# Performance work log

Hardware: AMD Instinct MI355X
Metric: run time of the kernel (lower is better)

The kernel has to match this reference:

```python
import jax, jax.numpy as jnp
import numpy as np

N_NODES = 100000
N_EDGES = 1600000
C = 128          # in_channels
H = 32           # hidden MLP width
D = 1            # Dirichlet concentration dims
T = 3            # Taylor params (estimate_bpr=True)
JITTER = 1e-20


def gcn_conv(x, W, b, edge_index, n_nodes):
    """PyG GCNConv: add self-loops, symmetric normalization, aggregate to target."""
    h = x @ W                                   # [N, C] transform first (smaller than gathering raw x then transforming per-edge)
    src = jnp.concatenate([edge_index[0], jnp.arange(n_nodes)])
    dst = jnp.concatenate([edge_index[1], jnp.arange(n_nodes)])
    deg = jax.ops.segment_sum(jnp.ones_like(dst, dtype=h.dtype), dst, num_segments=n_nodes)
    dinv = jnp.where(deg > 0, jax.lax.rsqrt(deg), 0.0)
    norm = dinv[src] * dinv[dst]                # [E+N]
    msg = h[src] * norm[:, None]                # gather + scale  [E+N, C]
    out = jax.ops.segment_sum(msg, dst, num_segments=n_nodes)  # scatter-add
    return out + b


def setup_inputs() -> dict:
    key = jax.random.key(0)
    ks = jax.random.split(key, 20)
    s = 1.0 / np.sqrt(C)
    sh = 1.0 / np.sqrt(H)
    x = jax.random.normal(ks[0], (N_NODES, C), dtype=jnp.float32)
    edge_index = jax.random.randint(ks[1], (2, N_EDGES), 0, N_NODES)
    p = {
        "x": x, "edge_index": edge_index,
        # actor params
        "a_conv_W": jax.random.uniform(ks[2], (C, C), jnp.float32, -s, s),
        "a_conv_b": jnp.zeros((C,), jnp.float32),
        "a_l1_W": jax.random.uniform(ks[3], (C, H), jnp.float32, -s, s),
        "a_l1_b": jax.random.uniform(ks[4], (H,), jnp.float32, -s, s),
        "a_l2_W": jax.random.uniform(ks[5], (H, H), jnp.float32, -sh, sh),
        "a_l2_b": jax.random.uniform(ks[6], (H,), jnp.float32, -sh, sh),
        "a_l3_W": jax.random.uniform(ks[7], (H, D + T), jnp.float32, -sh, sh),
        "a_l3_b": jax.random.uniform(ks[8], (D + T,), jnp.float32, -sh, sh),
        # critic params
        "c_conv_W": jax.random.uniform(ks[9], (C, C), jnp.float32, -s, s),
        "c_conv_b": jnp.zeros((C,), jnp.float32),
        "c_l1_W": jax.random.uniform(ks[10], (C, H), jnp.float32, -s, s),
        "c_l1_b": jax.random.uniform(ks[11], (H,), jnp.float32, -s, s),
        "c_l2_W": jax.random.uniform(ks[12], (H, H), jnp.float32, -sh, sh),
        "c_l2_b": jax.random.uniform(ks[13], (H,), jnp.float32, -sh, sh),
        "c_l3_W": jax.random.uniform(ks[14], (H, 1), jnp.float32, -sh, sh),
        "c_l3_b": jax.random.uniform(ks[15], (1,), jnp.float32, -sh, sh),
    }
    return p


def reference(x, edge_index,
              a_conv_W, a_conv_b, a_l1_W, a_l1_b, a_l2_W, a_l2_b, a_l3_W, a_l3_b,
              c_conv_W, c_conv_b, c_l1_W, c_l1_b, c_l2_W, c_l2_b, c_l3_W, c_l3_b):
    n = x.shape[0]
    # ---- actor (GNNActor.forward) ----
    a = jax.nn.relu(gcn_conv(x, a_conv_W, a_conv_b, edge_index, n)) + x   # residual
    a = jax.nn.relu(a @ a_l1_W + a_l1_b)
    a = jax.nn.relu(a @ a_l2_W + a_l2_b)
    a_out = a @ a_l3_W + a_l3_b                      # [N, D+T]
    concentration = jax.nn.softplus(a_out[:, :D]).reshape(-1) + JITTER
    taylor_params = jax.nn.softplus(a_out[:, D:]) + JITTER
    # ---- critic (GNNCritic.forward) ----
    c = jax.nn.relu(gcn_conv(x, c_conv_W, c_conv_b, edge_index, n)) + x
    c = jnp.sum(c, axis=0)                           # graph readout [C]
    c = jax.nn.relu(c @ c_l1_W + c_l1_b)
    c = jax.nn.relu(c @ c_l2_W + c_l2_b)
    value = c @ c_l3_W + c_l3_b                      # [1]
    return concentration, taylor_params, value
```

## Files before the change

### kernel.cpp

```cpp
#include <hip/hip_runtime.h>
#include <math.h>

#define CCH 128
#define HID 32
#define SLOTS 64
#define NBINS 391
#define BSHIFT 8
#define BCAP 4608

typedef __attribute__((ext_vector_type(8))) short bf16x8;
typedef __attribute__((ext_vector_type(4))) float f32x4;

__device__ __forceinline__ unsigned bf16pk(float a, float b) {
    unsigned ua = __builtin_bit_cast(unsigned, a);
    unsigned ub = __builtin_bit_cast(unsigned, b);
    ua = (ua + 0x7FFFu + ((ua >> 16) & 1u)) >> 16;
    ub = (ub + 0x7FFFu + ((ub >> 16) & 1u)) >> 16;
    return ua | (ub << 16);
}
__device__ __forceinline__ unsigned short bf16s(float a) {
    unsigned ua = __builtin_bit_cast(unsigned, a);
    ua = (ua + 0x7FFFu + ((ua >> 16) & 1u)) >> 16;
    return (unsigned short)ua;
}
__device__ __forceinline__ float bflo(unsigned v) {
    return __builtin_bit_cast(float, v << 16);
}
__device__ __forceinline__ float bfhi(unsigned v) {
    return __builtin_bit_cast(float, v & 0xFFFF0000u);
}

__global__ void k_zero(float* __restrict__ csum, int* __restrict__ binCnt) {
    int t = threadIdx.x;
    if (t < CCH) csum[t] = 0.f;
    for (int i = t; i < NBINS; i += 256) binCnt[i] = 0;
}

__global__ __launch_bounds__(256, 4)
void k_bin(const int* __restrict__ ei, int E,
           int* __restrict__ binCnt, unsigned* __restrict__ stage) {
    int t = threadIdx.x;
    __shared__ int lcnt[NBINS];
    __shared__ int lofs[NBINS];
    const int nchunk = (E + 2047) / 2048;
    for (int ch = blockIdx.x; ch < nchunk; ch += gridDim.x) {
        int base = ch * 2048;
        for (int i = t; i < NBINS; i += 256) lcnt[i] = 0;
        __syncthreads();
        unsigned pk[8]; int bin[8];
#pragma unroll
        for (int k = 0; k < 8; k++) {
            int e = base + k * 256 + t;
            if (e < E) {
                unsigned src = (unsigned)ei[e];
                unsigned dst = (unsigned)ei[E + e];
                bin[k] = dst >> BSHIFT;
                pk[k] = src | ((dst & 0xFFu) << 17);
                atomicAdd(&lcnt[bin[k]], 1);
            } else bin[k] = -1;
        }
        __syncthreads();
        for (int i = t; i < NBINS; i += 256) {
            int c = lcnt[i];
            lofs[i] = c ? atomicAdd(&binCnt[i], c) : 0;
        }
        __syncthreads();
#pragma unroll
        for (int k = 0; k < 8; k++) {
            if (bin[k] >= 0) {
                int pos = atomicAdd(&lofs[bin[k]], 1);
                if (pos < BCAP)
                    stage[(long)bin[k] * BCAP + pos] = pk[k];
            }
        }
        __syncthreads();
    }
}

__global__ __launch_bounds__(256)
void k_place(const unsigned* __restrict__ stage, const int* __restrict__ binCnt,
             int* __restrict__ cnt, int* __restrict__ csr) {
    __shared__ int lcnt[256];
    __shared__ int lofs[256];
    __shared__ int lcur[256];
    __shared__ int wtot[4];
    __shared__ unsigned ssrc[BCAP];
    __shared__ unsigned short sd8[BCAP];

    int t = threadIdx.x;
    int b = blockIdx.x;
    int count = binCnt[b];
    if (count > BCAP) count = BCAP;
    const unsigned* sp = stage + (long)b * BCAP;
    int dbase = b << BSHIFT;

    lcnt[t] = 0;
    __syncthreads();
    for (int i = t; i < count; i += 256)
        atomicAdd(&lcnt[sp[i] >> 17], 1);
    __syncthreads();

    int craw = lcnt[t];
    int cc = craw > SLOTS ? SLOTS : craw;
    int lane = t & 63, wv = t >> 6;
    int x = cc;
#pragma unroll
    for (int d = 1; d < 64; d <<= 1) {
        int y = __shfl_up(x, d, 64);
        if (lane >= d) x += y;
    }
    if (lane == 63) wtot[wv] = x;
    __syncthreads();
    int pre = 0;
#pragma unroll
    for (int k = 0; k < 4; k++) pre += (k < wv) ? wtot[k] : 0;
    int excl = pre + x - cc;
    lofs[t] = excl;
    lcur[t] = excl;
    int total = wtot[0] + wtot[1] + wtot[2] + wtot[3];
    __syncthreads();

    for (int i = t; i < count; i += 256) {
        unsigned p = sp[i];
        int d8 = (int)(p >> 17);
        int pos = atomicAdd(&lcur[d8], 1);
        if (pos - lofs[d8] < SLOTS) {
            ssrc[pos] = (p & 0x1FFFFu) << 5;
            sd8[pos] = (unsigned short)d8;
        }
    }
    __syncthreads();

    for (int i = t; i < total; i += 256) {
        int d8 = sd8[i];
        csr[(long)(dbase + d8) * SLOTS + (i - lofs[d8])] = (int)ssrc[i];
    }
    cnt[dbase + t] = craw;
}

__global__ __launch_bounds__(256, 4)
void k_prep(const float* __restrict__ aW, const float* __restrict__ cW,
            const float* __restrict__ x, const int* __restrict__ cnt,
            unsigned short* __restrict__ Wt, unsigned short* __restrict__ xsb,
            float* __restrict__ csum, int N) {
    __shared__ float scs[CCH];
    int t = threadIdx.x;
    int id = blockIdx.x * 256 + t;
    if (id < 32768) {
        int conv = id >> 14;
        int rem = id & 16383;
        int n = rem >> 7;
        int k = rem & 127;
        const float* W = conv ? cW : aW;
        Wt[id] = bf16s(W[k * CCH + n]);
    }
    if (blockIdx.x == 0 && t < 64) ((unsigned*)xsb)[(long)N * 64 + t] = 0u;

    const int n4 = N * 32;
    float c0 = 0.f, c1 = 0.f, c2 = 0.f, c3 = 0.f;
    const float4* x4 = (const float4*)x;
    uint2* xo = (uint2*)xsb;
    int stride = gridDim.x * 256;
    for (int i = id; i < n4; i += stride) {
        int node = i >> 5;
        float dv = rsqrtf((float)cnt[node] + 1.0f);
        float4 v = x4[i];
        c0 += v.x; c1 += v.y; c2 += v.z; c3 += v.w;
        uint2 p;
        p.x = bf16pk(dv * v.x, dv * v.y);
        p.y = bf16pk(dv * v.z, dv * v.w);
        xo[i] = p;
    }
    if (t < CCH) scs[t] = 0.f;
    __syncthreads();
    int c4 = (t & 31) * 4;
    atomicAdd(&scs[c4 + 0], c0);
    atomicAdd(&scs[c4 + 1], c1);
    atomicAdd(&scs[c4 + 2], c2);
    atomicAdd(&scs[c4 + 3], c3);
    __syncthreads();
    if (t < CCH) atomicAdd(&csum[t], scs[t]);
}

__global__ __launch_bounds__(256, 4)
void k_gather_y(const unsigned short* __restrict__ xs,
                const int* __restrict__ cnt,
                const int* __restrict__ csr,
                unsigned short* __restrict__ yb, int N) {
    int t = threadIdx.x;
    int lane = t & 63;
    int wid = t >> 6;
    int half = lane >> 5;
    int hl = lane & 31;
    int wg = blockIdx.x * 4 + wid;
    int stride = gridDim.x * 4;
    const uint2* xu = (const uint2*)xs;
    uint2* yu = (uint2*)yb;
    int npairs = N >> 1;
    int zoff = N << 5;

    for (int p = wg; p < npairs; p += stride) {
        int nA = p * 2;
        int degr = cnt[nA + half];
        float dvd = rsqrtf((float)degr + 1.0f);
        int deg = degr > SLOTS ? SLOTS : degr;
        int degA = __builtin_amdgcn_readlane(deg, 0);
        int degB = __builtin_amdgcn_readlane(deg, 32);
        int dmax = degA > degB ? degA : degB;
        dmax = __builtin_amdgcn_readfirstlane(dmax);

        int idxl = csr[(long)nA * SLOTS + lane + (lane & 32)];
        if (hl >= deg) idxl = zoff;

        uint2 vs = xu[(long)nA * 32 + lane];

        uint2 v[32];
#pragma unroll
        for (int e = 0; e < 32; e++) {
            int iA = __builtin_amdgcn_readlane(idxl, e);
            int iB = __builtin_amdgcn_readlane(idxl, 32 + e);
            int boff = half ? iB : iA;
            v[e] = xu[boff + hl];
        }

        float a0 = bflo(vs.x), a1 = bfhi(vs.x);
        float a2 = bflo(vs.y), a3 = bfhi(vs.y);
#pragma unroll
        for (int e = 0; e < 32; e++) {
            a0 += bflo(v[e].x);
            a1 += __builtin_bit_cast(float, v[e].x);
            a2 += bflo(v[e].y);
            a3 += __builtin_bit_cast(float, v[e].y);
        }

        if (dmax > 32) {
            int idxh = csr[(long)nA * SLOTS + lane + (lane & 32) + 32];
            if (hl + 32 >= deg) idxh = zoff;
            int dx8 = (dmax + 7) & ~7;
            for (int e = 32; e < dx8; e += 8) {
                uint2 w[8];
#pragma unroll
                for (int k = 0; k < 8; k++) {
                    int iA = __builtin_amdgcn_readlane(idxh, e - 32 + k);
                    int iB = __builtin_amdgcn_readlane(idxh, e + k);
                    int boff = half ? iB : iA;
                    w[k] = xu[boff + hl];
                }
#pragma unroll
                for (int k = 0; k < 8; k++) {
                    a0 += bflo(w[k].x);
                    a1 += __builtin_bit_cast(float, w[k].x);
                    a2 += bflo(w[k].y);
                    a3 += __builtin_bit_cast(float, w[k].y);
                }
            }
        }
        uint2 o;
        o.x = bf16pk(dvd * a0, dvd * a1);
        o.y = bf16pk(dvd * a2, dvd * a3);
        yu[(long)nA * 32 + lane] = o;
    }
}

__global__ __launch_bounds__(256, 4)
void k_gemm_y(const unsigned short* __restrict__ yb,
              const float* __restrict__ x,
              const unsigned short* __restrict__ Wt,
              const float* __restrict__ ab, const float* __restrict__ cb,
              unsigned short* __restrict__ a1b, float* __restrict__ csum,
              int N) {
    __shared__ unsigned short Ws[128 * 128];
    __shared__ float scs[CCH];
    int t = threadIdx.x;
    int row0 = blockIdx.x * 128;
    int wid = t >> 6, lane = t & 63;
    int m = lane & 15, quad = lane >> 4;
    int mrow0 = row0 + wid * 32;

    bf16x8 afr[2][4];
#pragma unroll
    for (int rt = 0; rt < 2; rt++) {
        int row = mrow0 + rt * 16 + m; if (row >= N) row = N - 1;
        const unsigned short* yr = yb + (long)row * CCH;
#pragma unroll
        for (int ks = 0; ks < 4; ks++)
            afr[rt][ks] = *(const bf16x8*)(yr + ks * 32 + quad * 8);
    }

    for (int conv = 0; conv < 2; conv++) {
        __syncthreads();
        const uint4* src = (const uint4*)(Wt + conv * 16384);
#pragma unroll
        for (int i = 0; i < 8; i++) {
            int id = i * 256 + t;
            int n = id >> 4, c = id & 15;
            uint4 v = src[id];
            *(uint4*)(Ws + n * 128 + ((c ^ (n & 15)) * 8)) = v;
        }
        if (conv == 1 && t < CCH) scs[t] = 0.f;
        __syncthreads();

#pragma unroll
        for (int nt = 0; nt < 8; nt++) {
            int n = nt * 16 + m;
            f32x4 ac0 = {0.f, 0.f, 0.f, 0.f};
            f32x4 ac1 = {0.f, 0.f, 0.f, 0.f};
#pragma unroll
            for (int ks = 0; ks < 4; ks++) {
                bf16x8 b = *(const bf16x8*)(Ws + n * 128 + (((ks * 4 + quad) ^ m) * 8));
                ac0 = __builtin_amdgcn_mfma_f32_16x16x32_bf16(afr[0][ks], b, ac0, 0, 0, 0);
                ac1 = __builtin_amdgcn_mfma_f32_16x16x32_bf16(afr[1][ks], b, ac1, 0, 0, 0);
            }
            float bias = conv ? cb[n] : ab[n];
            float part = 0.f;
#pragma unroll
            for (int h = 0; h < 2; h++) {
#pragma unroll
                for (int r = 0; r < 4; r++) {
                    int row = mrow0 + quad * 4 + r + h * 16;
                    float acv = h ? ac1[r] : ac0[r];
                    if (row < N) {
                        if (conv == 0) {
                            float xv = x[(long)row * CCH + n];
                            float v = fmaxf(acv + bias, 0.f) + xv;
                            a1b[(long)row * CCH + n] = bf16s(v);
                        } else {
                            part += fmaxf(acv + bias, 0.f);
                        }
                    }
                }
            }
            if (conv) atomicAdd(&scs[n], part);
        }
    }
    __syncthreads();
    if (t < CCH) atomicAdd(&csum[t], scs[t]);
}

__device__ __forceinline__ float softplus_f(float v) {
    return fmaxf(v, 0.f) + log1pf(expf(-fabsf(v)));
}

__global__ __launch_bounds__(256, 3)
void k_mlp(const unsigned short* __restrict__ a1b,
           const float* __restrict__ W1, const float* __restrict__ b1,
           const float* __restrict__ W2, const float* __restrict__ b2,
           const float* __restrict__ W3, const float* __restrict__ b3,
           const float* __restrict__ csum,
           const float* __restrict__ cW1, const float* __restrict__ cb1,
           const float* __restrict__ cW2, const float* __restrict__ cb2,
           const float* __restrict__ cW3, const float* __restrict__ cb3,
           float* __restrict__ out, int N) {
    __shared__ unsigned rowsW[64 * 65];
    __shared__ float h1L[64 * 33];
    __shared__ float h2L[64 * 33];
    int t = threadIdx.x;
    int l = t & 63;
    int w = t >> 6;
    long nbase = (long)blockIdx.x * 64;

    const uint4* ga = (const uint4*)(a1b + nbase * CCH);
#pragma unroll
    for (int i = 0; i < 4; i++) {
        int idx = i * 256 + t;
        int node = idx >> 4;
        int ch = idx & 15;
        uint4 v = make_uint4(0, 0, 0, 0);
        if (nbase + node < N) v = ga[node * 16 + ch];
        unsigned* dst = &rowsW[node * 65 + ch * 4];
        dst[0] = v.x; dst[1] = v.y; dst[2] = v.z; dst[3] = v.w;
    }
    __syncthreads();

    int j0 = __builtin_amdgcn_readfirstlane(w * 8);

    float h1[8];
#pragma unroll
    for (int j = 0; j < 8; j++) h1[j] = b1[j0 + j];
    for (int kp = 0; kp < 64; kp++) {
        unsigned v = rowsW[l * 65 + kp];
        float f0 = __builtin_bit_cast(float, v << 16);
        float f1 = __builtin_bit_cast(float, v & 0xFFFF0000u);
        const float* w0 = W1 + (2 * kp) * HID + j0;
        const float* w1 = W1 + (2 * kp + 1) * HID + j0;
#pragma unroll
        for (int j = 0; j < 8; j++)
            h1[j] = fmaf(f1, w1[j], fmaf(f0, w0[j], h1[j]));
    }
#pragma unroll
    for (int j = 0; j < 8; j++) h1L[l * 33 + j0 + j] = fmaxf(h1[j], 0.f);
    __syncthreads();

    float h2[8];
#pragma unroll
    for (int j = 0; j < 8; j++) h2[j] = b2[j0 + j];
    for (int k = 0; k < HID; k++) {
        float hv = h1L[l * 33 + k];
        const float* wr = W2 + k * HID + j0;
#pragma unroll
        for (int j = 0; j < 8; j++)
            h2[j] = fmaf(hv, wr[j], h2[j]);
    }
#pragma unroll
    for (int j = 0; j < 8; j++) h2L[l * 33 + j0 + j] = fmaxf(h2[j], 0.f);
    __syncthreads();

    if (w == 0) {
        long node = nbase + l;
        if (node < N) {
            float o[4] = {b3[0], b3[1], b3[2], b3[3]};
            for (int k = 0; k < HID; k++) {
                float hv = h2L[l * 33 + k];
#pragma unroll
                for (int m = 0; m < 4; m++)
                    o[m] = fmaf(hv, W3[k * 4 + m], o[m]);
            }
            out[node] = softplus_f(o[0]) + 1e-20f;
            float* ty = out + N;
            ty[node * 3 + 0] = softplus_f(o[1]) + 1e-20f;
            ty[node * 3 + 1] = softplus_f(o[2]) + 1e-20f;
            ty[node * 3 + 2] = softplus_f(o[3]) + 1e-20f;
        }
    }

    if (blockIdx.x == 0) {
        __syncthreads();
        float* cv  = h1L;
        float* hh1 = h2L;
        float* hh2 = h2L + 64;
        if (t < CCH) cv[t] = csum[t];
        __syncthreads();
        if (t < HID) {
            float a = cb1[t];
            for (int k = 0; k < CCH; k++) a = fmaf(cv[k], cW1[k * HID + t], a);
            hh1[t] = fmaxf(a, 0.f);
        }
        __syncthreads();
        if (t < HID) {
            float a = cb2[t];
            for (int k = 0; k < HID; k++) a = fmaf(hh1[k], cW2[k * HID + t], a);
            hh2[t] = fmaxf(a, 0.f);
        }
        __syncthreads();
        if (t == 0) {
            float a = cb3[0];
            for (int k = 0; k < HID; k++) a = fmaf(hh2[k], cW3[k], a);
            out[(long)4 * N] = a;
        }
    }
}

extern "C" void kernel_launch(void* const* d_in, const int* in_sizes, int n_in,
                              void* d_out, int out_size, void* d_ws, size_t ws_size,
                              hipStream_t stream) {
    const float* x   = (const float*)d_in[0];
    const int*   ei  = (const int*)d_in[1];
    const float* aW  = (const float*)d_in[2];
    const float* ab  = (const float*)d_in[3];
    const float* aW1 = (const float*)d_in[4];
    const float* ab1 = (const float*)d_in[5];
    const float* aW2 = (const float*)d_in[6];
    const float* ab2 = (const float*)d_in[7];
    const float* aW3 = (const float*)d_in[8];
    const float* ab3 = (const float*)d_in[9];
    const float* cW  = (const float*)d_in[10];
    const float* cb  = (const float*)d_in[11];
    const float* cW1 = (const float*)d_in[12];
    const float* cb1 = (const float*)d_in[13];
    const float* cW2 = (const float*)d_in[14];
    const float* cb2 = (const float*)d_in[15];
    const float* cW3 = (const float*)d_in[16];
    const float* cb3 = (const float*)d_in[17];
    float* out = (float*)d_out;

    const int N = in_sizes[0] / CCH;
    const int E = in_sizes[1] / 2;

    char* ws = (char*)d_ws;
    size_t off = 0;
    auto take = [&](size_t bytes) { void* p = ws + off; off += (bytes + 255) & ~(size_t)255; return p; };
    int*            cnt    = (int*)           take((size_t)NBINS * 256 * 4);
    int*            binCnt = (int*)           take(NBINS * 4);
    float*          csum   = (float*)         take(CCH * 4);
    unsigned short* Wt     = (unsigned short*)take(2 * 16384 * 2);
    int*            csr    = (int*)           take((size_t)N * SLOTS * 4);
    unsigned*       stage  = (unsigned*)      take((size_t)NBINS * BCAP * 4);
    unsigned short* xsb    = (unsigned short*)take((size_t)(N + 1) * CCH * 2);
    unsigned short* ybb    = (unsigned short*)take((size_t)N * CCH * 2);
    unsigned short* a1b    = (unsigned short*)take((size_t)N * CCH * 2);
    (void)ws_size;

    k_zero<<<1, 256, 0, stream>>>(csum, binCnt);
    k_bin<<<512, 256, 0, stream>>>(ei, E, binCnt, stage);
    k_place<<<NBINS, 256, 0, stream>>>(stage, binCnt, cnt, csr);

    k_prep<<<512, 256, 0, stream>>>(aW, cW, x, cnt, Wt, xsb, csum, N);

    k_gather_y<<<2048, 256, 0, stream>>>(xsb, cnt, csr, ybb, N);

    const int gblocks = (N + 127) / 128;
    k_gemm_y<<<gblocks, 256, 0, stream>>>(ybb, x, Wt, ab, cb, a1b, csum, N);

    k_mlp<<<(N + 63) / 64, 256, 0, stream>>>(a1b, aW1, ab1, aW2, ab2, aW3, ab3,
                                             csum, cW1, cb1, cW2, cb2, cW3, cb3,
                                             out, N);
}
```

Before: 336.7 us.

## Fuse node prep into placement kernel and make gather loop degree-bounded

Removes the separate k_prep launch. The weight transpose/bf16 conversion moves into k_zero, which now launches extra blocks. The degree-scaled bf16 conversion of x and the column sums move into k_place, so each bin's block converts its own 256 nodes using the degree counts already in shared memory. The gather kernel's first 32 neighbours now load in chunks of 8 up to the actual maximum degree instead of always issuing 32 loads. The trade-off is less memory-level parallelism in the gather and a longer k_place tail per block.

```diff
diff --git a/kernel.cpp b/kernel.cpp
--- a/kernel.cpp
+++ b/kernel.cpp
@@ -30,10 +30,24 @@
     return __builtin_bit_cast(float, v & 0xFFFF0000u);
 }
 
-__global__ void k_zero(float* __restrict__ csum, int* __restrict__ binCnt) {
+__global__ void k_zero(const float* __restrict__ aW, const float* __restrict__ cW,
+                       unsigned short* __restrict__ Wt,
+                       float* __restrict__ csum, int* __restrict__ binCnt,
+                       unsigned short* __restrict__ xsb, int N) {
     int t = threadIdx.x;
-    if (t < CCH) csum[t] = 0.f;
-    for (int i = t; i < NBINS; i += 256) binCnt[i] = 0;
+    if (blockIdx.x == 0) {
+        if (t < CCH) csum[t] = 0.f;
+        for (int i = t; i < NBINS; i += 256) binCnt[i] = 0;
+        if (t < 64) ((unsigned*)xsb)[(long)N * 64 + t] = 0u;
+        return;
+    }
+    int id = (blockIdx.x - 1) * 256 + t;
+    int conv = id >> 14;
+    int rem = id & 16383;
+    int n = rem >> 7;
+    int k = rem & 127;
+    const float* W = conv ? cW : aW;
+    Wt[id] = bf16s(W[k * CCH + n]);
 }
 
 __global__ __launch_bounds__(256, 4)
@@ -79,11 +93,14 @@
 
 __global__ __launch_bounds__(256)
 void k_place(const unsigned* __restrict__ stage, const int* __restrict__ binCnt,
-             int* __restrict__ cnt, int* __restrict__ csr) {
+             const float* __restrict__ x, int* __restrict__ cnt,
+             int* __restrict__ csr, unsigned short* __restrict__ xsb,
+             float* __restrict__ csum, int N) {
     __shared__ int lcnt[256];
     __shared__ int lofs[256];
     __shared__ int lcur[256];
     __shared__ int wtot[4];
+    __shared__ float scs[CCH];
     __shared__ unsigned ssrc[BCAP];
     __shared__ unsigned short sd8[BCAP];
 
@@ -103,21 +120,22 @@
     int craw = lcnt[t];
     int cc = craw > SLOTS ? SLOTS : craw;
     int lane = t & 63, wv = t >> 6;
-    int x = cc;
+    int xsc = cc;
 #pragma unroll
     for (int d = 1; d < 64; d <<= 1) {
-        int y = __shfl_up(x, d, 64);
-        if (lane >= d) x += y;
-    }
-    if (lane == 63) wtot[wv] = x;
+        int y = __shfl_up(xsc, d, 64);
+        if (lane >= d) xsc += y;
+    }
+    if (lane == 63) wtot[wv] = xsc;
     __syncthreads();
     int pre = 0;
 #pragma unroll
     for (int k = 0; k < 4; k++) pre += (k < wv) ? wtot[k] : 0;
-    int excl = pre + x - cc;
+    int excl = pre + xsc - cc;
     lofs[t] = excl;
     lcur[t] = excl;
     int total = wtot[0] + wtot[1] + wtot[2] + wtot[3];
+    cnt[dbase + t] = craw;
     __syncthreads();
 
     for (int i = t; i < count; i += 256) {
@@ -135,35 +153,14 @@
         int d8 = sd8[i];
         csr[(long)(dbase + d8) * SLOTS + (i - lofs[d8])] = (int)ssrc[i];
     }
-    cnt[dbase + t] = craw;
-}
-
-__global__ __launch_bounds__(256, 4)
-void k_prep(const float* __restrict__ aW, const float* __restrict__ cW,
-            const float* __restrict__ x, const int* __restrict__ cnt,
-            unsigned short* __restrict__ Wt, unsigned short* __restrict__ xsb,
-            float* __restrict__ csum, int N) {
-    __shared__ float scs[CCH];
-    int t = threadIdx.x;
-    int id = blockIdx.x * 256 + t;
-    if (id < 32768) {
-        int conv = id >> 14;
-        int rem = id & 16383;
-        int n = rem >> 7;
-        int k = rem & 127;
-        const float* W = conv ? cW : aW;
-        Wt[id] = bf16s(W[k * CCH + n]);
-    }
-    if (blockIdx.x == 0 && t < 64) ((unsigned*)xsb)[(long)N * 64 + t] = 0u;
-
-    const int n4 = N * 32;
+
+    int rows = N - dbase; if (rows > 256) rows = 256;
+    int nf4 = rows * 32;
+    const float4* x4 = (const float4*)(x + (long)dbase * CCH);
+    uint2* xo = (uint2*)xsb + (long)dbase * 32;
     float c0 = 0.f, c1 = 0.f, c2 = 0.f, c3 = 0.f;
-    const float4* x4 = (const float4*)x;
-    uint2* xo = (uint2*)xsb;
-    int stride = gridDim.x * 256;
-    for (int i = id; i < n4; i += stride) {
-        int node = i >> 5;
-        float dv = rsqrtf((float)cnt[node] + 1.0f);
+    for (int i = t; i < nf4; i += 256) {
+        float dv = rsqrtf((float)lcnt[i >> 5] + 1.0f);
         float4 v = x4[i];
         c0 += v.x; c1 += v.y; c2 += v.z; c3 += v.w;
         uint2 p;
@@ -213,26 +210,28 @@
         if (hl >= deg) idxl = zoff;
 
         uint2 vs = xu[(long)nA * 32 + lane];
-
-        uint2 v[32];
-#pragma unroll
-        for (int e = 0; e < 32; e++) {
-            int iA = __builtin_amdgcn_readlane(idxl, e);
-            int iB = __builtin_amdgcn_readlane(idxl, 32 + e);
-            int boff = half ? iB : iA;
-            v[e] = xu[boff + hl];
-        }
-
         float a0 = bflo(vs.x), a1 = bfhi(vs.x);
         float a2 = bflo(vs.y), a3 = bfhi(vs.y);
-#pragma unroll
-        for (int e = 0; e < 32; e++) {
-            a0 += bflo(v[e].x);
-            a1 += __builtin_bit_cast(float, v[e].x);
-            a2 += bflo(v[e].y);
-            a3 += __builtin_bit_cast(float, v[e].y);
-        }
-
+
+        int dm = dmax < 32 ? dmax : 32;
+        int dm8 = (dm + 7) & ~7;
+        for (int e = 0; e < dm8; e += 8) {
+            uint2 v[8];
+#pragma unroll
+            for (int k = 0; k < 8; k++) {
+                int iA = __builtin_amdgcn_readlane(idxl, e + k);
+                int iB = __builtin_amdgcn_readlane(idxl, 32 + e + k);
+                int boff = half ? iB : iA;
+                v[k] = xu[boff + hl];
+            }
+#pragma unroll
+            for (int k = 0; k < 8; k++) {
+                a0 += bflo(v[k].x);
+                a1 += __builtin_bit_cast(float, v[k].x);
+                a2 += bflo(v[k].y);
+                a3 += __builtin_bit_cast(float, v[k].y);
+            }
+        }
         if (dmax > 32) {
             int idxh = csr[(long)nA * SLOTS + lane + (lane & 32) + 32];
             if (hl + 32 >= deg) idxh = zoff;
@@ -490,11 +489,9 @@
     unsigned short* a1b    = (unsigned short*)take((size_t)N * CCH * 2);
     (void)ws_size;
 
-    k_zero<<<1, 256, 0, stream>>>(csum, binCnt);
+    k_zero<<<129, 256, 0, stream>>>(aW, cW, Wt, csum, binCnt, xsb, N);
     k_bin<<<512, 256, 0, stream>>>(ei, E, binCnt, stage);
-    k_place<<<NBINS, 256, 0, stream>>>(stage, binCnt, cnt, csr);
-
-    k_prep<<<512, 256, 0, stream>>>(aW, cW, x, cnt, Wt, xsb, csum, N);
+    k_place<<<NBINS, 256, 0, stream>>>(stage, binCnt, x, cnt, csr, xsb, csum, N);
 
     k_gather_y<<<2048, 256, 0, stream>>>(xsb, cnt, csr, ybb, N);
 
```

After: 337.8 us. About the same (+0.3%).
